# Performance work log

Hardware: AMD Instinct MI355X
Metric: run time of the kernel (lower is better)

The kernel has to match this reference:

```python
import jax, jax.numpy as jnp
import numpy as np

EPS = 1e-5

def _layernorm(h, g, b):
    m = h.mean(-1, keepdims=True)
    v = ((h - m) ** 2).mean(-1, keepdims=True)
    return (h - m) * jax.lax.rsqrt(v + EPS) * g + b

def _causal_conv(u, w, b):
    # u: (B,L,d), w: (d,K) depthwise, b: (d,)
    B, L, d = u.shape
    K = w.shape[-1]
    up = jnp.pad(u, ((0, 0), (K - 1, 0), (0, 0)))
    y = jnp.zeros_like(u) + b[None, None, :]
    for k in range(K):
        y = y + up[:, k:k + L, :] * w[:, k][None, None, :]
    return y

def _selective_scan(u, dt, Bm, Cm, A, Dv):
    # u, dt: (B,L,d); Bm, Cm: (B,L,N); A: (d,N); Dv: (d,)
    Bsz, L, d = u.shape
    N = A.shape[-1]

    def step(h, inp):
        dt_t, B_t, C_t, u_t = inp            # (B,d),(B,N),(B,N),(B,d)
        dA = jnp.exp(dt_t[..., None] * A)    # (B,d,N)
        h = dA * h + dt_t[..., None] * u_t[..., None] * B_t[:, None, :]
        y = jnp.einsum('bdn,bn->bd', h, C_t)
        return h, y

    h0 = jnp.zeros((Bsz, d, N), dtype=u.dtype)
    _, ys = jax.lax.scan(
        step, h0,
        (dt.transpose(1, 0, 2), Bm.transpose(1, 0, 2),
         Cm.transpose(1, 0, 2), u.transpose(1, 0, 2)))
    return ys.transpose(1, 0, 2) + u * Dv[None, None, :]

def _mamba_block(h, ipw, cw, cb, xpw, dtw, dtb, a_log, dv, opw, dt_rank, d_state):
    # h: (B,L,d_model)
    d_inner = dv.shape[0]
    xz = h @ ipw                              # (B,L,2*d_inner)
    u, z = xz[..., :d_inner], xz[..., d_inner:]
    u = jax.nn.silu(_causal_conv(u, cw, cb))
    proj = u @ xpw                            # (B,L,dt_rank+2N)
    dt_low = proj[..., :dt_rank]
    Bm = proj[..., dt_rank:dt_rank + d_state]
    Cm = proj[..., dt_rank + d_state:]
    dt = jax.nn.softplus(dt_low @ dtw + dtb)
    A = -jnp.exp(a_log)                       # (d_inner,N)
    y = _selective_scan(u, dt, Bm, Cm, A, dv)
    return (y * jax.nn.silu(z)) @ opw

def setup_inputs() -> dict:
    key = jax.random.key(0)
    ks = jax.random.split(key, 16)
    B, L = 8, 1024
    d_in, d_out, d_model = 3, 10, 256
    d_inner, N, K, nl, dt_rank = 512, 16, 4, 8, 16
    s = 0.02
    inp = {
        'x': jax.random.normal(ks[0], (B, d_in, L), dtype=jnp.float32),
        'enc_w': jax.random.normal(ks[1], (d_in, d_model)) * s,
        'enc_b': jnp.zeros((d_model,)),
        'in_proj_w': jax.random.normal(ks[2], (nl, d_model, 2 * d_inner)) * s,
        'conv_w': jax.random.normal(ks[3], (nl, d_inner, K)) * s,
        'conv_b': jnp.zeros((nl, d_inner)),
        'x_proj_w': jax.random.normal(ks[4], (nl, d_inner, dt_rank + 2 * N)) * s,
        'dt_w': jax.random.normal(ks[5], (nl, dt_rank, d_inner)) * s,
        'dt_b': jax.random.uniform(ks[6], (nl, d_inner), minval=-4.6, maxval=-2.3),
        'A_log': jnp.broadcast_to(
            jnp.log(jnp.arange(1, N + 1, dtype=jnp.float32)), (nl, d_inner, N)) + 0.0,
        'D': jnp.ones((nl, d_inner)),
        'out_proj_w': jax.random.normal(ks[7], (nl, d_inner, d_model)) * s,
        'ln_g': jnp.ones((nl, d_model)),
        'ln_b': jnp.zeros((nl, d_model)),
        'dec_w': jax.random.normal(ks[8], (d_model, d_out)) * s,
        'dec_b': jnp.zeros((d_out,)),
    }
    return inp

def reference(x, enc_w, enc_b, in_proj_w, conv_w, conv_b, x_proj_w,
              dt_w, dt_b, A_log, D, out_proj_w, ln_g, ln_b, dec_w, dec_b):
    dt_rank, d_state = dt_w.shape[1], A_log.shape[-1]
    nl = in_proj_w.shape[0]
    # (B, d_in, L) -> (B, L, d_in) -> encoder
    h = jnp.transpose(x, (0, 2, 1)) @ enc_w + enc_b   # (B,L,d_model)
    for i in range(nl):
        z = _mamba_block(h, in_proj_w[i], conv_w[i], conv_b[i], x_proj_w[i],
                         dt_w[i], dt_b[i], A_log[i], D[i], out_proj_w[i],
                         dt_rank, d_state)
        h = _layernorm(z + h, ln_g[i], ln_b[i])       # post-norm (prenorm=False)
    pooled = h.mean(axis=1)                           # (B,d_model)
    return pooled @ dec_w + dec_b
```

## Files before the change

kernel.cpp:

```cpp
#include <hip/hip_runtime.h>
#include <cstdint>
#include <cstddef>

#define DEV __device__ __forceinline__

typedef __attribute__((ext_vector_type(8))) short short8;
typedef __attribute__((ext_vector_type(4))) float f32x4;
typedef unsigned short u16;
typedef unsigned int u32;

constexpr int Bsz = 8, Lsz = 1024, DM = 256, DI = 512, NS = 16, DTR = 16;
constexpr int BL = Bsz * Lsz;
constexpr int NC = 64;
constexpr int SC = Lsz / NC;
constexpr int NL = 8;

constexpr size_t OFF_FLAGS = 0;
constexpr size_t OFF_H     = 256;
constexpr size_t SZ_H      = (size_t)BL * DM * 4;
constexpr size_t OFF_HBF   = OFF_H + SZ_H;
constexpr size_t SZ_HBF    = (size_t)BL * DM * 2;
constexpr size_t OFF_XZB   = OFF_HBF + SZ_HBF;
constexpr size_t SZ_XZB    = (size_t)BL * 1024 * 2;
constexpr size_t OFF_UC    = OFF_XZB + SZ_XZB;
constexpr size_t SZ_UC     = (size_t)BL * DI * 2;
constexpr size_t OFF_PRB   = OFF_UC + SZ_UC;
constexpr size_t SZ_PRB    = (size_t)BL * 64 * 2;
constexpr size_t OFF_HEND  = OFF_PRB + SZ_PRB;
constexpr size_t SZ_HEND   = (size_t)Bsz * NC * DI * NS * 2;
constexpr size_t OFF_DTS   = OFF_HEND + SZ_HEND;
constexpr size_t SZ_DTS    = (size_t)Bsz * NC * DI * 4;
constexpr size_t OFF_W1T   = OFF_DTS + SZ_DTS;
constexpr size_t SZ_W1T    = (size_t)NL * 1024 * 256 * 2;
constexpr size_t OFF_W2T   = OFF_W1T + SZ_W1T;
constexpr size_t SZ_W2T    = (size_t)NL * 64 * 512 * 2;
constexpr size_t OFF_W3T   = OFF_W2T + SZ_W2T;
constexpr size_t SZ_W3T    = (size_t)NL * 256 * 512 * 2;
constexpr size_t WS_NEED   = OFF_W3T + SZ_W3T;

DEV float bf2f(u16 v) {
  u32 x = ((u32)v) << 16;
  union { u32 u; float f; } c; c.u = x; return c.f;
}
DEV u16 f2bf(float f) {
  union { float f; u32 u; } c; c.f = f;
  u32 x = c.u;
  u32 r = (x + 0x7fffu + ((x >> 16) & 1u)) >> 16;
  return (u16)r;
}
DEV float fsigmoid(float x) { return 1.0f / (1.0f + __expf(-x)); }
DEV float loadf(const void* p, size_t idx, int isbf) {
  return isbf ? bf2f(((const u16*)p)[idx]) : ((const float*)p)[idx];
}

DEV void async16(const void* g, void* l) {
  __builtin_amdgcn_global_load_lds((const __attribute__((address_space(1))) u32*)g,
                                   (__attribute__((address_space(3))) u32*)l, 16, 0, 0);
}

__global__ __launch_bounds__(128)
void sentinel_k(u16* __restrict__ out) {
  if (threadIdx.x < 80) out[threadIdx.x] = 0x3F80u;
}

__global__ __launch_bounds__(64)
void probe_k(const u32* __restrict__ x, const u32* __restrict__ alog,
             const u32* __restrict__ Dv, const u32* __restrict__ dtb,
             const u32* __restrict__ w, int* __restrict__ flags) {
  int lane = threadIdx.x;
  u32 vx = x[lane], vw = w[lane];
  u32 ex = (vx >> 8) & 0x7F, ew = (vw >> 8) & 0x7F;
  unsigned long long mx = __ballot((ex >= 0x39 && ex <= 0x42) ? 1 : 0);
  unsigned long long mw = __ballot((ew >= 0x39 && ew <= 0x42) ? 1 : 0);
  int fa = (alog[0] != 0u) ? 1 : 0;
  float av = loadf(alog, 48 + (lane & 15), fa);
  int ok = fabsf(av - __logf((float)((lane & 15) + 1))) < 2e-3f ? 1 : 0;
  unsigned long long ms = __ballot(ok);
  if (lane == 0) {
    flags[0] = (__popcll(mx) >= 32) ? 1 : 0;
    flags[1] = fa;
    flags[2] = (Dv[0] == 0x3F803F80u) ? 1 : 0;
    flags[3] = ((((dtb[0] >> 8) & 0xFFu) == 0xC0u) &&
                (((dtb[1] >> 8) & 0xFFu) == 0xC0u)) ? 1 : 0;
    flags[4] = (__popcll(mw) >= 32) ? 1 : 0;
    flags[5] = (ms == ~0ull) ? 1 : 0;
  }
}

__global__ __launch_bounds__(256)
void transpose_pad_k(const void* __restrict__ in, u16* __restrict__ out,
                     int K, int N, int Npad, const int* __restrict__ flags) {
  int fw = flags[4];
  __shared__ u16 t[32][33];
  int k0 = blockIdx.x * 32, n0 = blockIdx.y * 32, z = blockIdx.z;
  size_t ibase = (size_t)z * K * N;
  out += (size_t)z * Npad * K;
  int tx = threadIdx.x, ty = threadIdx.y;
#pragma unroll
  for (int j = 0; j < 4; ++j) {
    int k = k0 + ty + j * 8, n = n0 + tx;
    t[ty + j * 8][tx] = (n < N) ? f2bf(loadf(in, ibase + (size_t)k * N + n, fw)) : (u16)0;
  }
  __syncthreads();
#pragma unroll
  for (int j = 0; j < 4; ++j) {
    int n = n0 + ty + j * 8, k = k0 + tx;
    out[(size_t)n * K + k] = t[tx][ty + j * 8];
  }
}

__global__ __launch_bounds__(256)
void encoder_k(const void* __restrict__ x, const void* __restrict__ ew,
               const u16* __restrict__ eb, float* __restrict__ h,
               u16* __restrict__ hbf, const int* __restrict__ flags) {
  int fx = flags[0], fw = flags[4];
  int bl = blockIdx.x, m = threadIdx.x;
  int b = bl >> 10, l = bl & 1023;
  float acc = bf2f(eb[m]);
#pragma unroll
  for (int c = 0; c < 3; ++c)
    acc += loadf(x, (size_t)(b * 3 + c) * 1024 + l, fx) * loadf(ew, c * 256 + m, fw);
  size_t idx = (size_t)bl * 256 + m;
  h[idx] = acc;
  hbf[idx] = f2bf(acc);
}

template<int BM, int BN, bool OUT16>
__global__ __launch_bounds__(256)
void gemm_bf16(const u16* __restrict__ A, const u16* __restrict__ Bt,
               void* __restrict__ Cv, int K) {
  constexpr int WTM = BM / 2, WTN = BN / 2;
  constexpr int MT = WTM / 16, NT = WTN / 16;
  constexpr int GA = BM * 4, GB = BN * 4;
  __shared__ __align__(16) u16 ldsA[BM * 32];
  __shared__ __align__(16) u16 ldsB[BN * 32];
  const int tid = threadIdx.x;
  const int wave = tid >> 6, lane = tid & 63;
  const int wr = wave >> 1, wc = wave & 1;
  const int q = lane >> 4, lr = lane & 15;
  const int m0 = blockIdx.x * BM, n0 = blockIdx.y * BN;
  const int ldc = gridDim.y * BN;

  f32x4 acc[MT][NT];
#pragma unroll
  for (int i = 0; i < MT; ++i)
#pragma unroll
    for (int j = 0; j < NT; ++j) acc[i][j] = (f32x4){0.f, 0.f, 0.f, 0.f};

  for (int kk = 0; kk < K; kk += 32) {
    __syncthreads();
    if constexpr (GA >= 256) {
#pragma unroll
      for (int rr = 0; rr < GA / 256; ++rr) {
        int i = tid + rr * 256;
        int row = i >> 2, s = i & 3, g = s ^ (row & 3);
        async16(A + (size_t)(m0 + row) * K + kk + g * 8, &ldsA[i * 8]);
      }
    } else {
      if (tid < GA) {
        int i = tid;
        int row = i >> 2, s = i & 3, g = s ^ (row & 3);
        async16(A + (size_t)(m0 + row) * K + kk + g * 8, &ldsA[i * 8]);
      }
    }
    if constexpr (GB >= 256) {
#pragma unroll
      for (int rr = 0; rr < GB / 256; ++rr) {
        int i = tid + rr * 256;
        int row = i >> 2, s = i & 3, g = s ^ (row & 3);
        async16(Bt + (size_t)(n0 + row) * K + kk + g * 8, &ldsB[i * 8]);
      }
    } else {
      if (tid < GB) {
        int i = tid;
        int row = i >> 2, s = i & 3, g = s ^ (row & 3);
        async16(Bt + (size_t)(n0 + row) * K + kk + g * 8, &ldsB[i * 8]);
      }
    }
    __syncthreads();

    short8 af[MT], bfr[NT];
#pragma unroll
    for (int mt = 0; mt < MT; ++mt) {
      int row = wr * WTM + mt * 16 + lr;
      int s = q ^ (row & 3);
      af[mt] = *(const short8*)&ldsA[row * 32 + s * 8];
    }
#pragma unroll
    for (int nt = 0; nt < NT; ++nt) {
      int row = wc * WTN + nt * 16 + lr;
      int s = q ^ (row & 3);
      bfr[nt] = *(const short8*)&ldsB[row * 32 + s * 8];
    }
#pragma unroll
    for (int mt = 0; mt < MT; ++mt)
#pragma unroll
      for (int nt = 0; nt < NT; ++nt)
        acc[mt][nt] = __builtin_amdgcn_mfma_f32_16x16x32_bf16(af[mt], bfr[nt], acc[mt][nt], 0, 0, 0);
  }
#pragma unroll
  for (int mt = 0; mt < MT; ++mt)
#pragma unroll
    for (int nt = 0; nt < NT; ++nt) {
      int col = n0 + wc * WTN + nt * 16 + lr;
      int row0 = m0 + wr * WTM + mt * 16 + q * 4;
#pragma unroll
      for (int i = 0; i < 4; ++i) {
        if (OUT16) ((u16*)Cv)[(size_t)(row0 + i) * ldc + col] = f2bf(acc[mt][nt][i]);
        else       ((float*)Cv)[(size_t)(row0 + i) * ldc + col] = acc[mt][nt][i];
      }
    }
}

#define UIDX(s, d) (((s) << 9) + (((((d) >> 3) ^ ((s) & 7))) << 3) + ((d) & 7))

DEV float dt_of(const u16* pr, const float* wv, float bias) {
  short8 d0 = *(const short8*)&pr[0];
  short8 d1 = *(const short8*)&pr[8];
  float xp = bias;
#pragma unroll
  for (int j = 0; j < 8; ++j) xp += bf2f((u16)d0[j]) * wv[j];
#pragma unroll
  for (int j = 0; j < 8; ++j) xp += bf2f((u16)d1[j]) * wv[8 + j];
  return __logf(1.f + __expf(fminf(xp, 30.f)));
}

__global__ __launch_bounds__(512, 4)
void fused_p1_k(const u16* __restrict__ xzb, const u16* __restrict__ w2t,
                const void* __restrict__ cw, const u16* __restrict__ cb,
                const void* __restrict__ alog, const void* __restrict__ dtw,
                const void* __restrict__ dtb,
                u16* __restrict__ uc, u16* __restrict__ prb,
                u16* __restrict__ hend, float* __restrict__ dts,
                const int* __restrict__ flags, int layer) {
  __shared__ __align__(16) u16 lds_x[16 * 512];
  __shared__ __align__(16) u16 lds_u[16 * 512];
  __shared__ __align__(16) u16 lds_p[16 * 64];
  const int fa = flags[1], fb = flags[3], fw = flags[4], fs = flags[5];
  const int tid = threadIdx.x;
  const int c = blockIdx.x, b = blockIdx.y;
  const int bl0 = b * 1024 + c * SC;
  const int l0 = c * SC;

#pragma unroll
  for (int rr = 0; rr < 2; ++rr) {
    int i = tid + rr * 512;
    int s = i >> 6, gcol = i & 63;
    async16(xzb + (size_t)(bl0 + s) * 1024 + gcol * 8, &lds_x[i * 8]);
  }
  float x0 = (l0 >= 3) ? bf2f(xzb[(size_t)(bl0 - 3) * 1024 + tid]) : 0.f;
  float x1 = (l0 >= 2) ? bf2f(xzb[(size_t)(bl0 - 2) * 1024 + tid]) : 0.f;
  float x2 = (l0 >= 1) ? bf2f(xzb[(size_t)(bl0 - 1) * 1024 + tid]) : 0.f;
  __syncthreads();

  {
    float cwv[4];
#pragma unroll
    for (int k = 0; k < 4; ++k) cwv[k] = loadf(cw, (size_t)layer * 2048 + tid * 4 + k, fw);
    float cbv = bf2f(cb[layer * 512 + tid]);
#pragma unroll
    for (int s = 0; s < SC; ++s) {
      float xn = bf2f(lds_x[s * 512 + tid]);
      float a = cbv + x0 * cwv[0] + x1 * cwv[1] + x2 * cwv[2] + xn * cwv[3];
      float uv = a * fsigmoid(a);
      u16 ub = f2bf(uv);
      lds_u[UIDX(s, tid)] = ub;
      uc[(size_t)(bl0 + s) * DI + tid] = ub;
      x0 = x1; x1 = x2; x2 = xn;
    }
  }
  __syncthreads();

  const int wave = tid >> 6, lane = tid & 63, q = lane >> 4, lr = lane & 15;
  if (wave < 4) {
    f32x4 acc = (f32x4){0.f, 0.f, 0.f, 0.f};
    const u16* bp = w2t + (size_t)(wave * 16 + lr) * 512 + q * 8;
#pragma unroll
    for (int kc = 0; kc < 16; ++kc) {
      short8 af = *(const short8*)&lds_u[UIDX(lr, kc * 32 + q * 8)];
      short8 bq8 = *(const short8*)&bp[kc * 32];
      acc = __builtin_amdgcn_mfma_f32_16x16x32_bf16(af, bq8, acc, 0, 0, 0);
    }
#pragma unroll
    for (int i = 0; i < 4; ++i) {
      u16 pv = f2bf(acc[i]);
      lds_p[(q * 4 + i) * 64 + wave * 16 + lr] = pv;
      prb[(size_t)(bl0 + q * 4 + i) * 64 + wave * 16 + lr] = pv;
    }
  }
  __syncthreads();

  float wv[16];
#pragma unroll
  for (int j = 0; j < 16; ++j)
    wv[j] = loadf(dtw, (size_t)layer * DTR * DI + (size_t)j * DI + tid, fw);
  float bias = loadf(dtb, (size_t)layer * DI + tid, fb);
  float An[16];
  if (!fs) {
    size_t aoff = (size_t)layer * DI * NS + (size_t)tid * NS;
#pragma unroll
    for (int j = 0; j < 16; ++j)
      An[j] = -__expf(fminf(loadf(alog, aoff + j, fa), 80.f));
  }
  float hh[16];
#pragma unroll
  for (int j = 0; j < 16; ++j) hh[j] = 0.f;
  float dsum = 0.f;
#pragma unroll 4
  for (int s = 0; s < SC; ++s) {
    const u16* pr = &lds_p[s * 64];
    float dt = dt_of(pr, wv, bias);
    float uv = bf2f(lds_u[UIDX(s, tid)]);
    float dtu = dt * uv;
    dsum += dt;
    short8 B0 = *(const short8*)&pr[16];
    short8 B1 = *(const short8*)&pr[24];
    if (fs) {
      float r = __expf(-dt), r2 = r * r;
      float pa = r, pb = r2;
#pragma unroll
      for (int i = 0; i < 4; ++i) {
        hh[2*i]   = pa * hh[2*i]   + dtu * bf2f((u16)B0[2*i]);
        hh[2*i+1] = pb * hh[2*i+1] + dtu * bf2f((u16)B0[2*i+1]);
        pa *= r2; pb *= r2;
      }
#pragma unroll
      for (int i = 0; i < 4; ++i) {
        hh[8+2*i] = pa * hh[8+2*i] + dtu * bf2f((u16)B1[2*i]);
        hh[9+2*i] = pb * hh[9+2*i] + dtu * bf2f((u16)B1[2*i+1]);
        pa *= r2; pb *= r2;
      }
    } else {
#pragma unroll
      for (int j = 0; j < 8; ++j) {
        hh[j]   = __expf(An[j]   * dt) * hh[j]   + dtu * bf2f((u16)B0[j]);
        hh[8+j] = __expf(An[8+j] * dt) * hh[8+j] + dtu * bf2f((u16)B1[j]);
      }
    }
  }
  size_t hbase = ((size_t)(b * NC + c) * DI + tid) * NS;
  short8 h0, h1;
#pragma unroll
  for (int j = 0; j < 8; ++j) { h0[j] = (short)f2bf(hh[j]); h1[j] = (short)f2bf(hh[8 + j]); }
  *(short8*)&hend[hbase] = h0;
  *(short8*)&hend[hbase + 8] = h1;
  dts[(size_t)(b * NC + c) * DI + tid] = dsum;
}

__global__ __launch_bounds__(256)
void scan_stitch_k(u16* hend_carry, const float* __restrict__ dts,
                   const void* __restrict__ alog, const int* __restrict__ flags,
                   int layer) {
  int fa = flags[1], fs = flags[5];
  int t = blockIdx.x * 256 + threadIdx.x;
  int b = t >> 13, dn = t & 8191;
  int d = dn >> 4, n = dn & 15;
  float An;
  if (fs) {
    An = -(float)(n + 1) * 1.44269504f;
  } else {
    float av = fminf(loadf(alog, (size_t)layer * DI * NS + d * NS + n, fa), 80.f);
    An = -__expf(av) * 1.44269504f;
  }
  float cv = 0.f;
#pragma unroll 8
  for (int c = 0; c < NC; ++c) {
    size_t ix = (size_t)(b * NC + c) * 8192 + dn;
    float a = exp2f(An * dts[(size_t)(b * NC + c) * DI + d]);
    float he = bf2f(hend_carry[ix]);
    hend_carry[ix] = f2bf(cv);
    cv = a * cv + he;
  }
}

__global__ __launch_bounds__(512, 4)
void fused_p3ln_k(const u16* __restrict__ prb, const u16* __restrict__ uc,
                  const u16* __restrict__ xzb, const u16* __restrict__ carry,
                  const void* __restrict__ alog, const void* __restrict__ dtw,
                  const void* __restrict__ dtb, const void* __restrict__ Dw,
                  const u16* __restrict__ w3t,
                  float* __restrict__ h, u16* __restrict__ hbf,
                  const void* __restrict__ g, const u16* __restrict__ bq,
                  const int* __restrict__ flags, int layer) {
  __shared__ __align__(16) u16 lds_p[16 * 64];
  __shared__ __align__(16) u16 lds_uc[16 * 512];
  __shared__ __align__(16) u16 lds_z[16 * 512];
  __shared__ __align__(16) u16 lds_g[16 * 512];
  __shared__ float ssum[16], ssq[16];
  const int fa = flags[1], fo = flags[2], fb = flags[3], fw = flags[4], fs = flags[5];
  const int tid = threadIdx.x;
  const int c = blockIdx.x, b = blockIdx.y;
  const int bl0 = b * 1024 + c * SC;

  if (tid < 128)
    async16(prb + (size_t)bl0 * 64 + tid * 8, &lds_p[tid * 8]);
#pragma unroll
  for (int rr = 0; rr < 2; ++rr) {
    int i = tid + rr * 512;
    int s = i >> 6, gcol = i & 63;
    async16(uc + (size_t)(bl0 + s) * DI + gcol * 8, &lds_uc[i * 8]);
  }
#pragma unroll
  for (int rr = 0; rr < 2; ++rr) {
    int i = tid + rr * 512;
    int s = i >> 6, gcol = i & 63;
    async16(xzb + (size_t)(bl0 + s) * 1024 + 512 + gcol * 8, &lds_z[i * 8]);
  }

  float wv[16];
#pragma unroll
  for (int j = 0; j < 16; ++j)
    wv[j] = loadf(dtw, (size_t)layer * DTR * DI + (size_t)j * DI + tid, fw);
  float bias = loadf(dtb, (size_t)layer * DI + tid, fb);
  float An[16];
  if (!fs) {
    size_t aoff = (size_t)layer * DI * NS + (size_t)tid * NS;
#pragma unroll
    for (int j = 0; j < 16; ++j)
      An[j] = -__expf(fminf(loadf(alog, aoff + j, fa), 80.f));
  }
  float Dv = loadf(Dw, (size_t)layer * DI + tid, fo);
  size_t hbase = ((size_t)(b * NC + c) * DI + tid) * NS;
  float hh[16];
  {
    short8 c0 = *(const short8*)&carry[hbase];
    short8 c1 = *(const short8*)&carry[hbase + 8];
#pragma unroll
    for (int j = 0; j < 8; ++j) { hh[j] = bf2f((u16)c0[j]); hh[8 + j] = bf2f((u16)c1[j]); }
  }
  __syncthreads();

#pragma unroll 4
  for (int s = 0; s < SC; ++s) {
    const u16* pr = &lds_p[s * 64];
    float dt = dt_of(pr, wv, bias);
    float uv = bf2f(lds_uc[s * 512 + tid]);
    float dtu = dt * uv;
    short8 B0 = *(const short8*)&pr[16];
    short8 B1 = *(const short8*)&pr[24];
    short8 C0 = *(const short8*)&pr[32];
    short8 C1 = *(const short8*)&pr[40];
    float ya = 0.f, yb = 0.f;
    if (fs) {
      float r = __expf(-dt), r2 = r * r;
      float pa = r, pb = r2;
#pragma unroll
      for (int i = 0; i < 4; ++i) {
        hh[2*i]   = pa * hh[2*i]   + dtu * bf2f((u16)B0[2*i]);   ya += hh[2*i]   * bf2f((u16)C0[2*i]);
        hh[2*i+1] = pb * hh[2*i+1] + dtu * bf2f((u16)B0[2*i+1]); yb += hh[2*i+1] * bf2f((u16)C0[2*i+1]);
        pa *= r2; pb *= r2;
      }
#pragma unroll
      for (int i = 0; i < 4; ++i) {
        hh[8+2*i] = pa * hh[8+2*i] + dtu * bf2f((u16)B1[2*i]);   ya += hh[8+2*i] * bf2f((u16)C1[2*i]);
        hh[9+2*i] = pb * hh[9+2*i] + dtu * bf2f((u16)B1[2*i+1]); yb += hh[9+2*i] * bf2f((u16)C1[2*i+1]);
        pa *= r2; pb *= r2;
      }
    } else {
#pragma unroll
      for (int j = 0; j < 8; ++j) {
        hh[j]   = __expf(An[j]   * dt) * hh[j]   + dtu * bf2f((u16)B0[j]);
        hh[8+j] = __expf(An[8+j] * dt) * hh[8+j] + dtu * bf2f((u16)B1[j]);
        if (j & 1) { yb += hh[j] * bf2f((u16)C0[j]); yb += hh[8+j] * bf2f((u16)C1[j]); }
        else       { ya += hh[j] * bf2f((u16)C0[j]); ya += hh[8+j] * bf2f((u16)C1[j]); }
      }
    }
    float y = (ya + yb) + uv * Dv;
    float z = bf2f(lds_z[s * 512 + tid]);
    float gg = y * z * fsigmoid(z);
    gg = fmaxf(-1e4f, fminf(1e4f, gg));
    lds_g[UIDX(s, tid)] = f2bf(gg);
  }
  __syncthreads();

  const int wave = tid >> 6, lane = tid & 63, q = lane >> 4, lr = lane & 15;
  f32x4 oacc[2];
  oacc[0] = (f32x4){0.f, 0.f, 0.f, 0.f};
  oacc[1] = (f32x4){0.f, 0.f, 0.f, 0.f};
  {
    const u16* w3b = w3t + (size_t)(wave * 32 + lr) * 512 + q * 8;
#pragma unroll
    for (int kc = 0; kc < 16; ++kc) {
      short8 af = *(const short8*)&lds_g[UIDX(lr, kc * 32 + q * 8)];
      short8 b0 = *(const short8*)&w3b[kc * 32];
      short8 b1 = *(const short8*)&w3b[16 * 512 + kc * 32];
      oacc[0] = __builtin_amdgcn_mfma_f32_16x16x32_bf16(af, b0, oacc[0], 0, 0, 0);
      oacc[1] = __builtin_amdgcn_mfma_f32_16x16x32_bf16(af, b1, oacc[1], 0, 0, 0);
    }
  }

  if (tid < 16) { ssum[tid] = 0.f; ssq[tid] = 0.f; }
  __syncthreads();
#pragma unroll
  for (int i = 0; i < 4; ++i) {
    int rowl = q * 4 + i;
    int row = bl0 + rowl;
    float pv = 0.f, pv2 = 0.f;
#pragma unroll
    for (int nt = 0; nt < 2; ++nt) {
      int col = wave * 32 + nt * 16 + lr;
      float v = oacc[nt][i] + h[(size_t)row * 256 + col];
      v = fmaxf(-1e15f, fminf(1e15f, v));
      oacc[nt][i] = v;
      pv += v; pv2 += v * v;
    }
#pragma unroll
    for (int o = 1; o <= 8; o <<= 1) {
      pv += __shfl_xor(pv, o);
      pv2 += __shfl_xor(pv2, o);
    }
    if (lr == 0) { atomicAdd(&ssum[rowl], pv); atomicAdd(&ssq[rowl], pv2); }
  }
  __syncthreads();
#pragma unroll
  for (int i = 0; i < 4; ++i) {
    int rowl = q * 4 + i;
    int row = bl0 + rowl;
    float mean = ssum[rowl] * (1.f / 256.f);
    float var = fmaxf(ssq[rowl] * (1.f / 256.f) - mean * mean, 0.f);
    float r = rsqrtf(var + 1e-5f);
#pragma unroll
    for (int nt = 0; nt < 2; ++nt) {
      int col = wave * 32 + nt * 16 + lr;
      float gv = loadf(g, (size_t)layer * DM + col, fo);
      float outv = (oacc[nt][i] - mean) * r * gv + bf2f(bq[layer * 256 + col]);
      size_t idx = (size_t)row * 256 + col;
      h[idx] = outv;
      hbf[idx] = f2bf(outv);
    }
  }
}

__global__ __launch_bounds__(256)
void pool_part_k(const float* __restrict__ h, float* __restrict__ part) {
  int c = blockIdx.x, b = blockIdx.y, m = threadIdx.x;
  const float* hp = h + ((size_t)(b * 1024 + c * 32)) * 256 + m;
  float s = 0.f;
#pragma unroll 8
  for (int l = 0; l < 32; ++l) s += hp[(size_t)l * 256];
  part[((size_t)(b * 32 + c)) * 256 + m] = s;
}

__global__ __launch_bounds__(256)
void pool_dec_k(const float* __restrict__ part, const void* __restrict__ dw,
                const u16* __restrict__ db, void* __restrict__ out,
                const int* __restrict__ flags) {
  int fx = flags[0], fw = flags[4];
  __shared__ float pool[256];
  int b = blockIdx.x, m = threadIdx.x;
  float s = 0.f;
#pragma unroll
  for (int c = 0; c < 32; ++c) s += part[((size_t)(b * 32 + c)) * 256 + m];
  pool[m] = s * (1.f / 1024.f);
  __syncthreads();
  if (m < 10) {
    float acc = bf2f(db[m]);
    for (int mm = 0; mm < 256; ++mm) acc += pool[mm] * loadf(dw, mm * 10 + m, fw);
    if (fx) ((u16*)out)[b * 10 + m] = f2bf(acc);
    else    ((float*)out)[b * 10 + m] = acc;
  }
}

extern "C" void kernel_launch(void* const* d_in, const int* in_sizes, int n_in,
                              void* d_out, int out_size, void* d_ws, size_t ws_size,
                              hipStream_t stream) {
  (void)in_sizes; (void)n_in; (void)out_size;
  if (ws_size < WS_NEED) {
    sentinel_k<<<1, 128, 0, stream>>>((u16*)d_out);
    return;
  }
  const void* x      = d_in[0];
  const void* enc_w  = d_in[1];
  const u16* enc_b   = (const u16*)d_in[2];
  const void* w_in   = d_in[3];
  const void* conv_w = d_in[4];
  const u16* conv_b  = (const u16*)d_in[5];
  const void* xpw    = d_in[6];
  const void* dtw    = d_in[7];
  const void* dtb    = d_in[8];
  const void* alog   = d_in[9];
  const void* Dw     = d_in[10];
  const void* opw    = d_in[11];
  const void* lng    = d_in[12];
  const u16* lnb     = (const u16*)d_in[13];
  const void* dcw    = d_in[14];
  const u16* dcb     = (const u16*)d_in[15];

  char* ws = (char*)d_ws;
  int*   flags = (int*)(ws + OFF_FLAGS);
  float* h    = (float*)(ws + OFF_H);
  u16*   hbf  = (u16*)(ws + OFF_HBF);
  u16*   xzb  = (u16*)(ws + OFF_XZB);
  u16*   uc   = (u16*)(ws + OFF_UC);
  u16*   prb  = (u16*)(ws + OFF_PRB);
  u16*   hend = (u16*)(ws + OFF_HEND);
  float* dts  = (float*)(ws + OFF_DTS);
  u16*   W1t  = (u16*)(ws + OFF_W1T);
  u16*   W2t  = (u16*)(ws + OFF_W2T);
  u16*   W3t  = (u16*)(ws + OFF_W3T);

  probe_k<<<1, 64, 0, stream>>>((const u32*)x, (const u32*)alog, (const u32*)Dw,
                                (const u32*)dtb, (const u32*)w_in, flags);

  transpose_pad_k<<<dim3(8, 32, 8),  dim3(32, 8), 0, stream>>>(w_in, W1t, 256, 1024, 1024, flags);
  transpose_pad_k<<<dim3(16, 2, 8),  dim3(32, 8), 0, stream>>>(xpw,  W2t, 512, 48,   64, flags);
  transpose_pad_k<<<dim3(16, 8, 8),  dim3(32, 8), 0, stream>>>(opw,  W3t, 512, 256,  256, flags);

  encoder_k<<<BL, 256, 0, stream>>>(x, enc_w, enc_b, h, hbf, flags);

  for (int i = 0; i < NL; ++i) {
    gemm_bf16<128, 128, true><<<dim3(BL / 128, 8), 256, 0, stream>>>(
        hbf, W1t + (size_t)i * 1024 * 256, xzb, 256);
    fused_p1_k<<<dim3(NC, Bsz), 512, 0, stream>>>(
        xzb, W2t + (size_t)i * 64 * 512, conv_w, conv_b, alog, dtw, dtb,
        uc, prb, hend, dts, flags, i);
    scan_stitch_k<<<Bsz * DI * NS / 256, 256, 0, stream>>>(hend, dts, alog, flags, i);
    fused_p3ln_k<<<dim3(NC, Bsz), 512, 0, stream>>>(
        prb, uc, xzb, hend, alog, dtw, dtb, Dw,
        W3t + (size_t)i * 256 * 512, h, hbf, lng, lnb, flags, i);
  }

  pool_part_k<<<dim3(32, Bsz), 256, 0, stream>>>(h, dts);
  pool_dec_k<<<Bsz, 256, 0, stream>>>(dts, dcw, dcb, d_out, flags);
}
```

Measured before the change: 747.2 us.

## Recompute conv in p3 instead of storing uc; fuse mean-pool into last layer

The p1 kernel no longer writes the post-conv activation u to global memory. The p3/LN kernel recomputes the causal conv and SiLU from the xz buffer, which removes a write and a read of a BL×512 bf16 tensor per layer at the cost of redundant conv math. The residual h rows are staged into LDS asynchronously, and the x_proj and out_proj weights are prefetched into registers ahead of the MFMA loops. The final mean-pool is folded into the last layer's epilogue via atomics into a small accumulator zeroed by the encoder, which drops the separate pool_part kernel but makes the float sum order nondeterministic.

```diff
diff --git a/kernel.cpp b/kernel.cpp
--- a/kernel.cpp
+++ b/kernel.cpp
@@ -22,9 +22,9 @@
 constexpr size_t SZ_HBF    = (size_t)BL * DM * 2;
 constexpr size_t OFF_XZB   = OFF_HBF + SZ_HBF;
 constexpr size_t SZ_XZB    = (size_t)BL * 1024 * 2;
-constexpr size_t OFF_UC    = OFF_XZB + SZ_XZB;
-constexpr size_t SZ_UC     = (size_t)BL * DI * 2;
-constexpr size_t OFF_PRB   = OFF_UC + SZ_UC;
+constexpr size_t OFF_PACC  = OFF_XZB + SZ_XZB;
+constexpr size_t SZ_PACC   = (size_t)Bsz * DM * 4;
+constexpr size_t OFF_PRB   = OFF_PACC + SZ_PACC;
 constexpr size_t SZ_PRB    = (size_t)BL * 64 * 2;
 constexpr size_t OFF_HEND  = OFF_PRB + SZ_PRB;
 constexpr size_t SZ_HEND   = (size_t)Bsz * NC * DI * NS * 2;
@@ -112,10 +112,12 @@
 __global__ __launch_bounds__(256)
 void encoder_k(const void* __restrict__ x, const void* __restrict__ ew,
                const u16* __restrict__ eb, float* __restrict__ h,
-               u16* __restrict__ hbf, const int* __restrict__ flags) {
+               u16* __restrict__ hbf, float* __restrict__ pacc,
+               const int* __restrict__ flags) {
   int fx = flags[0], fw = flags[4];
   int bl = blockIdx.x, m = threadIdx.x;
   int b = bl >> 10, l = bl & 1023;
+  if (bl < 8) pacc[bl * 256 + m] = 0.f;
   float acc = bf2f(eb[m]);
 #pragma unroll
   for (int c = 0; c < 3; ++c)
@@ -230,7 +232,7 @@
                 const void* __restrict__ cw, const u16* __restrict__ cb,
                 const void* __restrict__ alog, const void* __restrict__ dtw,
                 const void* __restrict__ dtb,
-                u16* __restrict__ uc, u16* __restrict__ prb,
+                u16* __restrict__ prb,
                 u16* __restrict__ hend, float* __restrict__ dts,
                 const int* __restrict__ flags, int layer) {
   __shared__ __align__(16) u16 lds_x[16 * 512];
@@ -241,6 +243,7 @@
   const int c = blockIdx.x, b = blockIdx.y;
   const int bl0 = b * 1024 + c * SC;
   const int l0 = c * SC;
+  const int wave = tid >> 6, lane = tid & 63, q = lane >> 4, lr = lane & 15;
 
 #pragma unroll
   for (int rr = 0; rr < 2; ++rr) {
@@ -248,6 +251,12 @@
     int s = i >> 6, gcol = i & 63;
     async16(xzb + (size_t)(bl0 + s) * 1024 + gcol * 8, &lds_x[i * 8]);
   }
+  const u16* bp = w2t + (size_t)((wave & 3) * 16 + lr) * 512 + q * 8;
+  short8 w2r[4];
+  if (wave < 4) {
+#pragma unroll
+    for (int p = 0; p < 4; ++p) w2r[p] = *(const short8*)&bp[p * 32];
+  }
   float x0 = (l0 >= 3) ? bf2f(xzb[(size_t)(bl0 - 3) * 1024 + tid]) : 0.f;
   float x1 = (l0 >= 2) ? bf2f(xzb[(size_t)(bl0 - 2) * 1024 + tid]) : 0.f;
   float x2 = (l0 >= 1) ? bf2f(xzb[(size_t)(bl0 - 1) * 1024 + tid]) : 0.f;
@@ -263,22 +272,19 @@
       float xn = bf2f(lds_x[s * 512 + tid]);
       float a = cbv + x0 * cwv[0] + x1 * cwv[1] + x2 * cwv[2] + xn * cwv[3];
       float uv = a * fsigmoid(a);
-      u16 ub = f2bf(uv);
-      lds_u[UIDX(s, tid)] = ub;
-      uc[(size_t)(bl0 + s) * DI + tid] = ub;
+      lds_u[UIDX(s, tid)] = f2bf(uv);
       x0 = x1; x1 = x2; x2 = xn;
     }
   }
   __syncthreads();
 
-  const int wave = tid >> 6, lane = tid & 63, q = lane >> 4, lr = lane & 15;
   if (wave < 4) {
     f32x4 acc = (f32x4){0.f, 0.f, 0.f, 0.f};
-    const u16* bp = w2t + (size_t)(wave * 16 + lr) * 512 + q * 8;
 #pragma unroll
     for (int kc = 0; kc < 16; ++kc) {
       short8 af = *(const short8*)&lds_u[UIDX(lr, kc * 32 + q * 8)];
-      short8 bq8 = *(const short8*)&bp[kc * 32];
+      short8 bq8 = w2r[kc & 3];
+      if (kc < 12) w2r[kc & 3] = *(const short8*)&bp[(kc + 4) * 32];
       acc = __builtin_amdgcn_mfma_f32_16x16x32_bf16(af, bq8, acc, 0, 0, 0);
     }
 #pragma unroll
@@ -374,31 +380,33 @@
 }
 
 __global__ __launch_bounds__(512, 4)
-void fused_p3ln_k(const u16* __restrict__ prb, const u16* __restrict__ uc,
-                  const u16* __restrict__ xzb, const u16* __restrict__ carry,
+void fused_p3ln_k(const u16* __restrict__ xzb, const u16* __restrict__ prb,
+                  const u16* __restrict__ carry,
+                  const void* __restrict__ cw, const u16* __restrict__ cb,
                   const void* __restrict__ alog, const void* __restrict__ dtw,
                   const void* __restrict__ dtb, const void* __restrict__ Dw,
                   const u16* __restrict__ w3t,
                   float* __restrict__ h, u16* __restrict__ hbf,
+                  float* __restrict__ pacc,
                   const void* __restrict__ g, const u16* __restrict__ bq,
-                  const int* __restrict__ flags, int layer) {
+                  const int* __restrict__ flags, int layer, int last) {
+  __shared__ __align__(16) u16 lds_x[16 * 512];
+  __shared__ __align__(16) u16 lds_z[16 * 512];
+  __shared__ __align__(16) u16 lds_ug[16 * 512];
   __shared__ __align__(16) u16 lds_p[16 * 64];
-  __shared__ __align__(16) u16 lds_uc[16 * 512];
-  __shared__ __align__(16) u16 lds_z[16 * 512];
-  __shared__ __align__(16) u16 lds_g[16 * 512];
   __shared__ float ssum[16], ssq[16];
   const int fa = flags[1], fo = flags[2], fb = flags[3], fw = flags[4], fs = flags[5];
   const int tid = threadIdx.x;
   const int c = blockIdx.x, b = blockIdx.y;
   const int bl0 = b * 1024 + c * SC;
-
-  if (tid < 128)
-    async16(prb + (size_t)bl0 * 64 + tid * 8, &lds_p[tid * 8]);
+  const int l0 = c * SC;
+  const int wave = tid >> 6, lane = tid & 63, q = lane >> 4, lr = lane & 15;
+
 #pragma unroll
   for (int rr = 0; rr < 2; ++rr) {
     int i = tid + rr * 512;
     int s = i >> 6, gcol = i & 63;
-    async16(uc + (size_t)(bl0 + s) * DI + gcol * 8, &lds_uc[i * 8]);
+    async16(xzb + (size_t)(bl0 + s) * 1024 + gcol * 8, &lds_x[i * 8]);
   }
 #pragma unroll
   for (int rr = 0; rr < 2; ++rr) {
@@ -406,7 +414,16 @@
     int s = i >> 6, gcol = i & 63;
     async16(xzb + (size_t)(bl0 + s) * 1024 + 512 + gcol * 8, &lds_z[i * 8]);
   }
-
+  if (tid < 128)
+    async16(prb + (size_t)bl0 * 64 + tid * 8, &lds_p[tid * 8]);
+
+  float x0 = (l0 >= 3) ? bf2f(xzb[(size_t)(bl0 - 3) * 1024 + tid]) : 0.f;
+  float x1 = (l0 >= 2) ? bf2f(xzb[(size_t)(bl0 - 2) * 1024 + tid]) : 0.f;
+  float x2 = (l0 >= 1) ? bf2f(xzb[(size_t)(bl0 - 1) * 1024 + tid]) : 0.f;
+  float cwv[4];
+#pragma unroll
+  for (int k = 0; k < 4; ++k) cwv[k] = loadf(cw, (size_t)layer * 2048 + tid * 4 + k, fw);
+  float cbv = bf2f(cb[layer * 512 + tid]);
   float wv[16];
 #pragma unroll
   for (int j = 0; j < 16; ++j)
@@ -430,11 +447,35 @@
   }
   __syncthreads();
 
+#pragma unroll
+  for (int s = 0; s < SC; ++s) {
+    float xn = bf2f(lds_x[s * 512 + tid]);
+    float a = cbv + x0 * cwv[0] + x1 * cwv[1] + x2 * cwv[2] + xn * cwv[3];
+    float uv = a * fsigmoid(a);
+    lds_ug[UIDX(s, tid)] = f2bf(uv);
+    x0 = x1; x1 = x2; x2 = xn;
+  }
+  __syncthreads();
+
+#pragma unroll
+  for (int rr = 0; rr < 2; ++rr) {
+    int i = tid + rr * 512;
+    int row = i >> 6, gcol = i & 63;
+    async16(h + (size_t)(bl0 + row) * 256 + gcol * 4, &((float*)lds_x)[i * 4]);
+  }
+  const u16* w3b = w3t + (size_t)(wave * 32 + lr) * 512 + q * 8;
+  short8 r0[4], r1[4];
+#pragma unroll
+  for (int p = 0; p < 4; ++p) {
+    r0[p] = *(const short8*)&w3b[p * 32];
+    r1[p] = *(const short8*)&w3b[16 * 512 + p * 32];
+  }
+
 #pragma unroll 4
   for (int s = 0; s < SC; ++s) {
     const u16* pr = &lds_p[s * 64];
     float dt = dt_of(pr, wv, bias);
-    float uv = bf2f(lds_uc[s * 512 + tid]);
+    float uv = bf2f(lds_ug[UIDX(s, tid)]);
     float dtu = dt * uv;
     short8 B0 = *(const short8*)&pr[16];
     short8 B1 = *(const short8*)&pr[24];
@@ -469,37 +510,36 @@
     float z = bf2f(lds_z[s * 512 + tid]);
     float gg = y * z * fsigmoid(z);
     gg = fmaxf(-1e4f, fminf(1e4f, gg));
-    lds_g[UIDX(s, tid)] = f2bf(gg);
-  }
-  __syncthreads();
-
-  const int wave = tid >> 6, lane = tid & 63, q = lane >> 4, lr = lane & 15;
+    lds_ug[UIDX(s, tid)] = f2bf(gg);
+  }
+  __syncthreads();
+
   f32x4 oacc[2];
   oacc[0] = (f32x4){0.f, 0.f, 0.f, 0.f};
   oacc[1] = (f32x4){0.f, 0.f, 0.f, 0.f};
-  {
-    const u16* w3b = w3t + (size_t)(wave * 32 + lr) * 512 + q * 8;
-#pragma unroll
-    for (int kc = 0; kc < 16; ++kc) {
-      short8 af = *(const short8*)&lds_g[UIDX(lr, kc * 32 + q * 8)];
-      short8 b0 = *(const short8*)&w3b[kc * 32];
-      short8 b1 = *(const short8*)&w3b[16 * 512 + kc * 32];
-      oacc[0] = __builtin_amdgcn_mfma_f32_16x16x32_bf16(af, b0, oacc[0], 0, 0, 0);
-      oacc[1] = __builtin_amdgcn_mfma_f32_16x16x32_bf16(af, b1, oacc[1], 0, 0, 0);
-    }
+#pragma unroll
+  for (int kc = 0; kc < 16; ++kc) {
+    short8 af = *(const short8*)&lds_ug[UIDX(lr, kc * 32 + q * 8)];
+    short8 b0 = r0[kc & 3], b1 = r1[kc & 3];
+    if (kc < 12) {
+      r0[kc & 3] = *(const short8*)&w3b[(kc + 4) * 32];
+      r1[kc & 3] = *(const short8*)&w3b[16 * 512 + (kc + 4) * 32];
+    }
+    oacc[0] = __builtin_amdgcn_mfma_f32_16x16x32_bf16(af, b0, oacc[0], 0, 0, 0);
+    oacc[1] = __builtin_amdgcn_mfma_f32_16x16x32_bf16(af, b1, oacc[1], 0, 0, 0);
   }
 
   if (tid < 16) { ssum[tid] = 0.f; ssq[tid] = 0.f; }
   __syncthreads();
+  const float* hres = (const float*)lds_x;
 #pragma unroll
   for (int i = 0; i < 4; ++i) {
     int rowl = q * 4 + i;
-    int row = bl0 + rowl;
     float pv = 0.f, pv2 = 0.f;
 #pragma unroll
     for (int nt = 0; nt < 2; ++nt) {
       int col = wave * 32 + nt * 16 + lr;
-      float v = oacc[nt][i] + h[(size_t)row * 256 + col];
+      float v = oacc[nt][i] + hres[rowl * 256 + col];
       v = fmaxf(-1e15f, fminf(1e15f, v));
       oacc[nt][i] = v;
       pv += v; pv2 += v * v;
@@ -512,6 +552,7 @@
     if (lr == 0) { atomicAdd(&ssum[rowl], pv); atomicAdd(&ssq[rowl], pv2); }
   }
   __syncthreads();
+  float ps0 = 0.f, ps1 = 0.f;
 #pragma unroll
   for (int i = 0; i < 4; ++i) {
     int rowl = q * 4 + i;
@@ -527,31 +568,27 @@
       size_t idx = (size_t)row * 256 + col;
       h[idx] = outv;
       hbf[idx] = f2bf(outv);
+      if (nt == 0) ps0 += outv; else ps1 += outv;
+    }
+  }
+  if (last) {
+    ps0 += __shfl_xor(ps0, 16); ps0 += __shfl_xor(ps0, 32);
+    ps1 += __shfl_xor(ps1, 16); ps1 += __shfl_xor(ps1, 32);
+    if (q == 0) {
+      atomicAdd(&pacc[b * 256 + wave * 32 + lr], ps0);
+      atomicAdd(&pacc[b * 256 + wave * 32 + 16 + lr], ps1);
     }
   }
 }
 
 __global__ __launch_bounds__(256)
-void pool_part_k(const float* __restrict__ h, float* __restrict__ part) {
-  int c = blockIdx.x, b = blockIdx.y, m = threadIdx.x;
-  const float* hp = h + ((size_t)(b * 1024 + c * 32)) * 256 + m;
-  float s = 0.f;
-#pragma unroll 8
-  for (int l = 0; l < 32; ++l) s += hp[(size_t)l * 256];
-  part[((size_t)(b * 32 + c)) * 256 + m] = s;
-}
-
-__global__ __launch_bounds__(256)
-void pool_dec_k(const float* __restrict__ part, const void* __restrict__ dw,
+void pool_dec_k(const float* __restrict__ pacc, const void* __restrict__ dw,
                 const u16* __restrict__ db, void* __restrict__ out,
                 const int* __restrict__ flags) {
   int fx = flags[0], fw = flags[4];
   __shared__ float pool[256];
   int b = blockIdx.x, m = threadIdx.x;
-  float s = 0.f;
-#pragma unroll
-  for (int c = 0; c < 32; ++c) s += part[((size_t)(b * 32 + c)) * 256 + m];
-  pool[m] = s * (1.f / 1024.f);
+  pool[m] = pacc[b * 256 + m] * (1.f / 1024.f);
   __syncthreads();
   if (m < 10) {
     float acc = bf2f(db[m]);
@@ -591,7 +628,7 @@
   float* h    = (float*)(ws + OFF_H);
   u16*   hbf  = (u16*)(ws + OFF_HBF);
   u16*   xzb  = (u16*)(ws + OFF_XZB);
-  u16*   uc   = (u16*)(ws + OFF_UC);
+  float* pacc = (float*)(ws + OFF_PACC);
   u16*   prb  = (u16*)(ws + OFF_PRB);
   u16*   hend = (u16*)(ws + OFF_HEND);
   float* dts  = (float*)(ws + OFF_DTS);
@@ -606,20 +643,20 @@
   transpose_pad_k<<<dim3(16, 2, 8),  dim3(32, 8), 0, stream>>>(xpw,  W2t, 512, 48,   64, flags);
   transpose_pad_k<<<dim3(16, 8, 8),  dim3(32, 8), 0, stream>>>(opw,  W3t, 512, 256,  256, flags);
 
-  encoder_k<<<BL, 256, 0, stream>>>(x, enc_w, enc_b, h, hbf, flags);
+  encoder_k<<<BL, 256, 0, stream>>>(x, enc_w, enc_b, h, hbf, pacc, flags);
 
   for (int i = 0; i < NL; ++i) {
     gemm_bf16<128, 128, true><<<dim3(BL / 128, 8), 256, 0, stream>>>(
         hbf, W1t + (size_t)i * 1024 * 256, xzb, 256);
     fused_p1_k<<<dim3(NC, Bsz), 512, 0, stream>>>(
         xzb, W2t + (size_t)i * 64 * 512, conv_w, conv_b, alog, dtw, dtb,
-        uc, prb, hend, dts, flags, i);
+        prb, hend, dts, flags, i);
     scan_stitch_k<<<Bsz * DI * NS / 256, 256, 0, stream>>>(hend, dts, alog, flags, i);
     fused_p3ln_k<<<dim3(NC, Bsz), 512, 0, stream>>>(
-        prb, uc, xzb, hend, alog, dtw, dtb, Dw,
-        W3t + (size_t)i * 256 * 512, h, hbf, lng, lnb, flags, i);
-  }
-
-  pool_part_k<<<dim3(32, Bsz), 256, 0, stream>>>(h, dts);
-  pool_dec_k<<<Bsz, 256, 0, stream>>>(dts, dcw, dcb, d_out, flags);
-}
+        xzb, prb, hend, conv_w, conv_b, alog, dtw, dtb, Dw,
+        W3t + (size_t)i * 256 * 512, h, hbf, pacc, lng, lnb, flags, i,
+        (i == NL - 1) ? 1 : 0);
+  }
+
+  pool_dec_k<<<Bsz, 256, 0, stream>>>(pacc, dcw, dcb, d_out, flags);
+}
```

Result: no change. 736.4 us (-1.4%).
